# Performance work log

Hardware: AMD Instinct MI355X
Metric: run time of the kernel (lower is better)

The kernel has to match this reference:

```python
import jax, jax.numpy as jnp
import numpy as np

C_IN, C_OUT, KH, KW = 64, 128, 3, 3
STRIDE, PAD, DIL = 1, 1, 1
EPS = 1e-5


def setup_inputs() -> dict:
    key = jax.random.key(0)
    ks = jax.random.split(key, 7)
    B, H, W = 8, 112, 112
    x = jax.random.normal(ks[0], (B, C_IN, H, W), dtype=jnp.float32)
    # offset conv: produces 2*KH*KW offset channels; small init keeps offsets sane
    w_off = jax.random.normal(ks[1], (2 * KH * KW, C_IN, KH, KW), dtype=jnp.float32) * 0.01
    b_off = jax.random.normal(ks[2], (2 * KH * KW,), dtype=jnp.float32) * 0.01
    # deformable conv weight/bias
    fan_in = C_IN * KH * KW
    w_dcn = jax.random.normal(ks[3], (C_OUT, C_IN, KH, KW), dtype=jnp.float32) / np.sqrt(fan_in)
    b_dcn = jax.random.normal(ks[4], (C_OUT,), dtype=jnp.float32) * 0.01
    gamma = jnp.ones((C_OUT,), dtype=jnp.float32)
    beta = jnp.zeros((C_OUT,), dtype=jnp.float32)
    return {"x": x, "w_off": w_off, "b_off": b_off, "w_dcn": w_dcn,
            "b_dcn": b_dcn, "gamma": gamma, "beta": beta}


def _conv2d(x, w, b):
    y = jax.lax.conv_general_dilated(
        x, w, window_strides=(STRIDE, STRIDE),
        padding=((PAD, PAD), (PAD, PAD)),
        rhs_dilation=(DIL, DIL),
        dimension_numbers=("NCHW", "OIHW", "NCHW"))
    return y + b[None, :, None, None]


def _deform_conv(x, offset, w, b):
    # x: [B,C,H,W]; offset: [B, 2*KH*KW, Ho, Wo] with (dy, dx) pairs per tap
    B, C, H, W = x.shape
    KK = KH * KW
    Ho, Wo = offset.shape[2], offset.shape[3]
    off = offset.reshape(B, KK, 2, Ho, Wo)
    ky = (jnp.arange(KK) // KW).astype(jnp.float32)  # kernel row per tap
    kx = (jnp.arange(KK) % KW).astype(jnp.float32)
    base_y = (jnp.arange(Ho) * STRIDE - PAD).astype(jnp.float32)
    base_x = (jnp.arange(Wo) * STRIDE - PAD).astype(jnp.float32)
    # sampling positions [B, KK, Ho, Wo]
    py = off[:, :, 0] + base_y[None, None, :, None] + (ky * DIL)[None, :, None, None]
    px = off[:, :, 1] + base_x[None, None, None, :] + (kx * DIL)[None, :, None, None]

    y0 = jnp.floor(py)
    x0 = jnp.floor(px)
    wy1 = py - y0  # weight for y0+1
    wx1 = px - x0
    y0i = y0.astype(jnp.int32)
    x0i = x0.astype(jnp.int32)

    x_flat = x.reshape(B, C, H * W)

    def gather_corner(yi, xi, wgt):
        # yi, xi, wgt: [B, KK, Ho, Wo]
        valid = (yi >= 0) & (yi < H) & (xi >= 0) & (xi < W)
        idx = jnp.clip(yi, 0, H - 1) * W + jnp.clip(xi, 0, W - 1)
        idx = idx.reshape(B, -1)  # [B, KK*Ho*Wo]
        vals = jnp.take_along_axis(x_flat, idx[:, None, :], axis=2)  # [B, C, N]
        coef = (wgt * valid.astype(wgt.dtype)).reshape(B, 1, -1)
        return vals * coef

    samp = (gather_corner(y0i,     x0i,     (1 - wy1) * (1 - wx1))
            + gather_corner(y0i,     x0i + 1, (1 - wy1) * wx1)
            + gather_corner(y0i + 1, x0i,     wy1 * (1 - wx1))
            + gather_corner(y0i + 1, x0i + 1, wy1 * wx1))
    samp = samp.reshape(B, C, KK, Ho, Wo)
    out = jnp.einsum("bckhw,ock->bohw", samp, w.reshape(w.shape[0], C, KK))
    return out + b[None, :, None, None]


def reference(x, w_off, b_off, w_dcn, b_dcn, gamma, beta):
    offset = _conv2d(x, w_off, b_off)
    y = _deform_conv(x, offset, w_dcn, b_dcn)
    # BatchNorm2d (training mode: biased batch stats) + ReLU
    mean = jnp.mean(y, axis=(0, 2, 3))
    var = jnp.var(y, axis=(0, 2, 3))
    yhat = (y - mean[None, :, None, None]) * jax.lax.rsqrt(var + EPS)[None, :, None, None]
    y = gamma[None, :, None, None] * yhat + beta[None, :, None, None]
    return jax.nn.relu(y)
```

## Files before the change

kernel.cpp:

```cpp
#include <hip/hip_runtime.h>

#define H    112
#define W    112
#define HW   12544
#define CIN  64
#define COUT 128
#define BATCH 8
#define KK   9
#define OFFC 18
#define EPS  1e-5f
#define TP   32
#define KDIM 576
#define KHALF 288
#define KPAD2 296
#define NB   3136

typedef unsigned short ushort;
typedef unsigned int uint;
typedef _Float16 half2v __attribute__((ext_vector_type(2)));
typedef _Float16 half8  __attribute__((ext_vector_type(8)));
typedef __attribute__((ext_vector_type(4))) float floatx4;

__device__ __forceinline__ half2v u2h(uint u) {
  union { uint u; half2v h; } c; c.u = u; return c.h;
}
__device__ __forceinline__ uint h2u(half2v h) {
  union { uint u; half2v h; } c; c.h = h; return c.u;
}
__device__ __forceinline__ uint pack_h2(float a, float b) {
  half2v h; h[0] = (_Float16)a; h[1] = (_Float16)b; return h2u(h);
}
__device__ __forceinline__ ushort f2h_bits(float v) {
  union { _Float16 h; ushort u; } c; c.h = (_Float16)v; return c.u;
}

__global__ __launch_bounds__(256) void k_transpose_x(
    const float* __restrict__ x, ushort* __restrict__ xTh) {
  __shared__ float tile[64][65];
  int b = blockIdx.y;
  int p0 = blockIdx.x * 64;
  int tid = threadIdx.x;
  int j = tid & 63, cb = tid >> 6;
#pragma unroll
  for (int i = 0; i < 16; ++i) {
    int ci = cb * 16 + i;
    tile[ci][j] = x[((size_t)(b * CIN + ci)) * HW + p0 + j];
  }
  __syncthreads();
  int px = tid >> 2, ciq = tid & 3;
#pragma unroll
  for (int g = 0; g < 4; ++g) {
    int ci = ciq * 16 + g * 4;
    uint lo = pack_h2(tile[ci + 0][px], tile[ci + 1][px]);
    uint hi = pack_h2(tile[ci + 2][px], tile[ci + 3][px]);
    *(uint2*)&xTh[((size_t)b * HW + p0 + px) * 64 + ci] = make_uint2(lo, hi);
  }
}

__global__ __launch_bounds__(256) void k_prep_w(
    const float* __restrict__ w_off, const float* __restrict__ w_dcn,
    ushort* __restrict__ w_offT, ushort* __restrict__ w_mf) {
  int i = blockIdx.x * 256 + threadIdx.x;
  if (i < 32 * KDIM) {
    int oc = i / KDIM, k = i - oc * KDIM;
    int kk = k >> 6, ci = k & 63;
    float v = (oc < OFFC) ? w_off[(oc * CIN + ci) * KK + kk] : 0.f;
    w_offT[i] = f2h_bits(v);
  } else if (i < 32 * KDIM + COUT * KDIM) {
    int jj = i - 32 * KDIM;
    int co = jj / KDIM, k = jj - co * KDIM;
    int h = k / KHALF, r = k - h * KHALF;
    int kk = r >> 5, cil = r & 31;
    int ci = h * 32 + cil;
    w_mf[jj] = f2h_bits(w_dcn[(co * CIN + ci) * KK + kk]);
  }
}

__global__ __launch_bounds__(256) void k_offset_conv(
    const ushort* __restrict__ xTh, const ushort* __restrict__ w_offT,
    const float* __restrict__ bias, float* __restrict__ out) {
  int b = blockIdx.y;
  int wave = threadIdx.x >> 6, lane = threadIdx.x & 63;
  int row16 = lane & 15, quad = lane >> 4;
  int p = blockIdx.x * 64 + wave * 16 + row16;
  int ho = p / W, wo = p - ho * W;
  const ushort* xb = xTh + (size_t)b * HW * 64;

  half8 Bf[18];
#pragma unroll
  for (int ks = 0; ks < 18; ++ks) {
    int kk = ks >> 1;
    int ci0 = (ks & 1) * 32 + quad * 8;
    int kh = kk / 3, kw = kk - kh * 3;
    int yy = ho + kh - 1, xx = wo + kw - 1;
    bool valid = (yy >= 0) & (yy < H) & (xx >= 0) & (xx < W);
    half8 v = {0, 0, 0, 0, 0, 0, 0, 0};
    if (valid) v = *(const half8*)(xb + ((size_t)(yy * W + xx) << 6) + ci0);
    Bf[ks] = v;
  }
  floatx4 acc0 = {0.f, 0.f, 0.f, 0.f}, acc1 = acc0;
  const ushort* wa0 = w_offT + row16 * KDIM + quad * 8;
  const ushort* wa1 = w_offT + (16 + row16) * KDIM + quad * 8;
#pragma unroll
  for (int ks = 0; ks < 18; ++ks) {
    half8 A0 = *(const half8*)(wa0 + ks * 32);
    half8 A1 = *(const half8*)(wa1 + ks * 32);
    acc0 = __builtin_amdgcn_mfma_f32_16x16x32_f16(A0, Bf[ks], acc0, 0, 0, 0);
    acc1 = __builtin_amdgcn_mfma_f32_16x16x32_f16(A1, Bf[ks], acc1, 0, 0, 0);
  }
  float* ob = out + (size_t)b * OFFC * HW;
#pragma unroll
  for (int reg = 0; reg < 4; ++reg) {
    int oc = quad * 4 + reg;
    ob[(size_t)oc * HW + p] = acc0[reg] + bias[oc];
    int oc1 = 16 + oc;
    if (oc1 < OFFC) ob[(size_t)oc1 * HW + p] = acc1[reg] + bias[oc1];
  }
}

__global__ __launch_bounds__(256) void k_deform(
    const ushort* __restrict__ xTh, const float* __restrict__ off,
    const ushort* __restrict__ w_mf, float* __restrict__ y,
    float* __restrict__ psT) {
  __shared__ uint4  s_wh[KK][TP];
  __shared__ int4   s_i[KK][TP];
  __shared__ ushort samp[TP][KPAD2];

  int b = blockIdx.y;
  int p0 = blockIdx.x * TP;
  int bid = blockIdx.y * gridDim.x + blockIdx.x;
  int tid = threadIdx.x;
  const ushort* xb = xTh + (size_t)b * HW * 64;

  for (int it = tid; it < KK * TP; it += 256) {
    int kk = it >> 5;
    int px = it & 31;
    int p = p0 + px;
    int ho = p / W, wo = p - ho * W;
    float dy = off[((size_t)b * OFFC + 2 * kk) * HW + p];
    float dx = off[((size_t)b * OFFC + 2 * kk + 1) * HW + p];
    float py = dy + (float)(ho - 1 + kk / 3);
    float pxx = dx + (float)(wo - 1 + kk % 3);
    float y0f = floorf(py), x0f = floorf(pxx);
    float wy1 = py - y0f, wx1 = pxx - x0f;
    int y0 = (int)y0f, x0 = (int)x0f;
    int y1 = y0 + 1, x1 = x0 + 1;
    float vy0 = (y0 >= 0 && y0 < H) ? 1.f : 0.f;
    float vy1 = (y1 >= 0 && y1 < H) ? 1.f : 0.f;
    float vx0 = (x0 >= 0 && x0 < W) ? 1.f : 0.f;
    float vx1 = (x1 >= 0 && x1 < W) ? 1.f : 0.f;
    int cy0 = min(max(y0, 0), H - 1), cy1 = min(max(y1, 0), H - 1);
    int cx0 = min(max(x0, 0), W - 1), cx1 = min(max(x1, 0), W - 1);
    float w00 = (1.f - wy1) * (1.f - wx1) * vy0 * vx0;
    float w01 = (1.f - wy1) * wx1 * vy0 * vx1;
    float w10 = wy1 * (1.f - wx1) * vy1 * vx0;
    float w11 = wy1 * wx1 * vy1 * vx1;
    s_wh[kk][px] = make_uint4(pack_h2(w00, w00), pack_h2(w01, w01),
                              pack_h2(w10, w10), pack_h2(w11, w11));
    s_i[kk][px] = make_int4((cy0 * W + cx0) << 6, (cy0 * W + cx1) << 6,
                            (cy1 * W + cx0) << 6, (cy1 * W + cx1) << 6);
  }
  __syncthreads();

  int wave = tid >> 6, lane = tid & 63;
  int row16 = lane & 15, quad = lane >> 4;
  int koff = quad * 8;
  int co_base = wave * 32;
  const ushort* wa0 = w_mf + (size_t)(co_base + row16) * KDIM + koff;
  const ushort* wa1 = w_mf + (size_t)(co_base + 16 + row16) * KDIM + koff;

  floatx4 acc00 = {0.f, 0.f, 0.f, 0.f}, acc01 = acc00, acc10 = acc00, acc11 = acc00;

  for (int h = 0; h < 2; ++h) {
#pragma unroll
    for (int r = 0; r < 5; ++r) {
      int it = tid + r * 256;
      if (it < 1152) {
        int px = it / 36;
        int rem = it - px * 36;
        int kk = rem >> 2;
        int cig = rem & 3;
        int cil0 = cig * 8;
        int cio = h * 32 + cil0;
        uint4 wh = s_wh[kk][px];
        int4 iv = s_i[kk][px];
        half2v w0 = u2h(wh.x), w1 = u2h(wh.y), w2 = u2h(wh.z), w3 = u2h(wh.w);
        uint4 c0 = *(const uint4*)(xb + iv.x + cio);
        uint4 c1 = *(const uint4*)(xb + iv.y + cio);
        uint4 c2 = *(const uint4*)(xb + iv.z + cio);
        uint4 c3 = *(const uint4*)(xb + iv.w + cio);
        uint4 res;
        res.x = h2u(w0 * u2h(c0.x) + w1 * u2h(c1.x) + w2 * u2h(c2.x) + w3 * u2h(c3.x));
        res.y = h2u(w0 * u2h(c0.y) + w1 * u2h(c1.y) + w2 * u2h(c2.y) + w3 * u2h(c3.y));
        res.z = h2u(w0 * u2h(c0.z) + w1 * u2h(c1.z) + w2 * u2h(c2.z) + w3 * u2h(c3.z));
        res.w = h2u(w0 * u2h(c0.w) + w1 * u2h(c1.w) + w2 * u2h(c2.w) + w3 * u2h(c3.w));
        *(uint4*)&samp[px][kk * 32 + cil0] = res;
      }
    }
    __syncthreads();

    const ushort* sb0 = &samp[row16][koff];
    const ushort* sb1 = &samp[16 + row16][koff];
    const ushort* a0 = wa0 + h * KHALF;
    const ushort* a1 = wa1 + h * KHALF;
#pragma unroll
    for (int ks = 0; ks < 9; ++ks) {
      half8 A0 = *(const half8*)(a0 + ks * 32);
      half8 A1 = *(const half8*)(a1 + ks * 32);
      half8 B0 = *(const half8*)(sb0 + ks * 32);
      half8 B1 = *(const half8*)(sb1 + ks * 32);
      acc00 = __builtin_amdgcn_mfma_f32_16x16x32_f16(A0, B0, acc00, 0, 0, 0);
      acc01 = __builtin_amdgcn_mfma_f32_16x16x32_f16(A0, B1, acc01, 0, 0, 0);
      acc10 = __builtin_amdgcn_mfma_f32_16x16x32_f16(A1, B0, acc10, 0, 0, 0);
      acc11 = __builtin_amdgcn_mfma_f32_16x16x32_f16(A1, B1, acc11, 0, 0, 0);
    }
    if (h == 0) __syncthreads();
  }

  float* yb = y + (size_t)b * COUT * HW + p0;
#pragma unroll
  for (int reg = 0; reg < 4; ++reg) {
    int r0 = quad * 4 + reg;
    yb[(size_t)(co_base + r0) * HW + row16]      = acc00[reg];
    yb[(size_t)(co_base + r0) * HW + 16 + row16] = acc01[reg];
    yb[(size_t)(co_base + 16 + r0) * HW + row16]      = acc10[reg];
    yb[(size_t)(co_base + 16 + r0) * HW + 16 + row16] = acc11[reg];
  }
#pragma unroll
  for (int reg = 0; reg < 4; ++reg) {
    float s0 = acc00[reg] + acc01[reg];
    float q0 = acc00[reg] * acc00[reg] + acc01[reg] * acc01[reg];
    float s1 = acc10[reg] + acc11[reg];
    float q1 = acc10[reg] * acc10[reg] + acc11[reg] * acc11[reg];
#pragma unroll
    for (int m = 1; m < 16; m <<= 1) {
      s0 += __shfl_xor(s0, m, 64);
      q0 += __shfl_xor(q0, m, 64);
      s1 += __shfl_xor(s1, m, 64);
      q1 += __shfl_xor(q1, m, 64);
    }
    if (row16 == 0) {
      int c0 = co_base + quad * 4 + reg;
      int c1 = c0 + 16;
      psT[(size_t)c0 * NB + bid]         = s0;
      psT[(size_t)(128 + c0) * NB + bid] = q0;
      psT[(size_t)c1 * NB + bid]         = s1;
      psT[(size_t)(128 + c1) * NB + bid] = q1;
    }
  }
}

__global__ __launch_bounds__(256) void k_reduce(const float* __restrict__ psT,
                                                float* __restrict__ stats) {
  int j = blockIdx.x;
  int tid = threadIdx.x;
  float s = 0.f;
  for (int i = tid; i < NB; i += 256) s += psT[(size_t)j * NB + i];
#pragma unroll
  for (int o = 32; o > 0; o >>= 1) s += __shfl_down(s, o, 64);
  __shared__ float ls[4];
  int lane = tid & 63, wid = tid >> 6;
  if (lane == 0) ls[wid] = s;
  __syncthreads();
  if (tid == 0) stats[j] = ls[0] + ls[1] + ls[2] + ls[3];
}

__global__ __launch_bounds__(256) void k_norm(const float* __restrict__ y,
                                              const float* __restrict__ stats,
                                              const float* __restrict__ gamma,
                                              const float* __restrict__ beta,
                                              float* __restrict__ out) {
  int i4 = blockIdx.x * 256 + threadIdx.x;
  const int total4 = BATCH * COUT * HW / 4;
  if (i4 >= total4) return;
  size_t i = (size_t)i4 * 4;
  int c = (int)((i / HW) & (COUT - 1));
  const float N = (float)(BATCH * HW);
  float m = stats[c] / N;
  float var = stats[COUT + c] / N - m * m;
  float r = rsqrtf(var + EPS);
  float g = gamma[c], bt = beta[c];
  float4 v = *(const float4*)&y[i];
  v.x = fmaxf(0.f, (v.x - m) * r * g + bt);
  v.y = fmaxf(0.f, (v.y - m) * r * g + bt);
  v.z = fmaxf(0.f, (v.z - m) * r * g + bt);
  v.w = fmaxf(0.f, (v.w - m) * r * g + bt);
  *(float4*)&out[i] = v;
}

extern "C" void kernel_launch(void* const* d_in, const int* in_sizes, int n_in,
                              void* d_out, int out_size, void* d_ws, size_t ws_size,
                              hipStream_t stream) {
  const float* x     = (const float*)d_in[0];
  const float* w_off = (const float*)d_in[1];
  const float* b_off = (const float*)d_in[2];
  const float* w_dcn = (const float*)d_in[3];
  const float* gamma = (const float*)d_in[5];
  const float* beta  = (const float*)d_in[6];
  float* out = (float*)d_out;

  float* ws = (float*)d_ws;
  float*  off_buf = ws;
  float*  psT     = off_buf + 1806336;
  float*  stats   = psT + 802816;
  float*  y       = stats + 256;
  ushort* xTh     = (ushort*)(y + 12845056);
  ushort* w_mf    = xTh + 6422528;
  ushort* w_offT  = w_mf + 73728;

  k_transpose_x<<<dim3(HW / 64, BATCH), 256, 0, stream>>>(x, xTh);
  k_prep_w<<<(32 * KDIM + COUT * KDIM + 255) / 256, 256, 0, stream>>>(w_off, w_dcn, w_offT, w_mf);
  k_offset_conv<<<dim3(HW / 64, BATCH), 256, 0, stream>>>(xTh, w_offT, b_off, off_buf);
  k_deform<<<dim3(HW / TP, BATCH), 256, 0, stream>>>(xTh, off_buf, w_mf, y, psT);
  k_reduce<<<256, 256, 0, stream>>>(psT, stats);
  k_norm<<<(BATCH * COUT * HW / 4 + 255) / 256, 256, 0, stream>>>(y, stats, gamma, beta, out);
}
```

Measured before the change: 238.9 us.

## Store deform-conv output as fp16 via LDS-staged coalesced writes; restructure stats reduction

The deform kernel now stages its accumulator tile through shared memory, which is unioned with the sampling buffers, and writes the pre-norm activations as fp16 with vectorized coalesced stores instead of scattered fp32 stores. Per-block BN partial sums are also staged in shared memory and written contiguously. The reduce kernel now uses atomics over a block-major layout, which needs a memset of the stats buffer first. The norm kernel reads fp16 and processes eight elements per thread. This roughly halves intermediate traffic, at the cost of fp16 rounding of the pre-norm values and non-deterministic atomic summation order.

```diff
diff --git a/kernel.cpp b/kernel.cpp
--- a/kernel.cpp
+++ b/kernel.cpp
@@ -14,6 +14,7 @@
 #define KHALF 288
 #define KPAD2 296
 #define NB   3136
+#define YPAD 36
 
 typedef unsigned short ushort;
 typedef unsigned int uint;
@@ -32,6 +33,9 @@
 }
 __device__ __forceinline__ ushort f2h_bits(float v) {
   union { _Float16 h; ushort u; } c; c.h = (_Float16)v; return c.u;
+}
+__device__ __forceinline__ float h2f_bits(ushort u) {
+  union { ushort u; _Float16 h; } c; c.u = u; return (float)c.h;
 }
 
 __global__ __launch_bounds__(256) void k_transpose_x(
@@ -118,13 +122,15 @@
   }
 }
 
+struct SMemA { uint4 s_wh[KK][TP]; int4 s_i[KK][TP]; ushort samp[TP][KPAD2]; };
+struct SMemB { ushort yst[COUT][YPAD]; float stat_s[COUT]; float stat_q[COUT]; };
+union SMemU { SMemA a; SMemB b; };
+
 __global__ __launch_bounds__(256) void k_deform(
     const ushort* __restrict__ xTh, const float* __restrict__ off,
-    const ushort* __restrict__ w_mf, float* __restrict__ y,
+    const ushort* __restrict__ w_mf, ushort* __restrict__ y,
     float* __restrict__ psT) {
-  __shared__ uint4  s_wh[KK][TP];
-  __shared__ int4   s_i[KK][TP];
-  __shared__ ushort samp[TP][KPAD2];
+  __shared__ SMemU sm;
 
   int b = blockIdx.y;
   int p0 = blockIdx.x * TP;
@@ -155,10 +161,10 @@
     float w01 = (1.f - wy1) * wx1 * vy0 * vx1;
     float w10 = wy1 * (1.f - wx1) * vy1 * vx0;
     float w11 = wy1 * wx1 * vy1 * vx1;
-    s_wh[kk][px] = make_uint4(pack_h2(w00, w00), pack_h2(w01, w01),
-                              pack_h2(w10, w10), pack_h2(w11, w11));
-    s_i[kk][px] = make_int4((cy0 * W + cx0) << 6, (cy0 * W + cx1) << 6,
-                            (cy1 * W + cx0) << 6, (cy1 * W + cx1) << 6);
+    sm.a.s_wh[kk][px] = make_uint4(pack_h2(w00, w00), pack_h2(w01, w01),
+                                   pack_h2(w10, w10), pack_h2(w11, w11));
+    sm.a.s_i[kk][px] = make_int4((cy0 * W + cx0) << 6, (cy0 * W + cx1) << 6,
+                                 (cy1 * W + cx0) << 6, (cy1 * W + cx1) << 6);
   }
   __syncthreads();
 
@@ -182,8 +188,8 @@
         int cig = rem & 3;
         int cil0 = cig * 8;
         int cio = h * 32 + cil0;
-        uint4 wh = s_wh[kk][px];
-        int4 iv = s_i[kk][px];
+        uint4 wh = sm.a.s_wh[kk][px];
+        int4 iv = sm.a.s_i[kk][px];
         half2v w0 = u2h(wh.x), w1 = u2h(wh.y), w2 = u2h(wh.z), w3 = u2h(wh.w);
         uint4 c0 = *(const uint4*)(xb + iv.x + cio);
         uint4 c1 = *(const uint4*)(xb + iv.y + cio);
@@ -194,13 +200,13 @@
         res.y = h2u(w0 * u2h(c0.y) + w1 * u2h(c1.y) + w2 * u2h(c2.y) + w3 * u2h(c3.y));
         res.z = h2u(w0 * u2h(c0.z) + w1 * u2h(c1.z) + w2 * u2h(c2.z) + w3 * u2h(c3.z));
         res.w = h2u(w0 * u2h(c0.w) + w1 * u2h(c1.w) + w2 * u2h(c2.w) + w3 * u2h(c3.w));
-        *(uint4*)&samp[px][kk * 32 + cil0] = res;
+        *(uint4*)&sm.a.samp[px][kk * 32 + cil0] = res;
       }
     }
     __syncthreads();
 
-    const ushort* sb0 = &samp[row16][koff];
-    const ushort* sb1 = &samp[16 + row16][koff];
+    const ushort* sb0 = &sm.a.samp[row16][koff];
+    const ushort* sb1 = &sm.a.samp[16 + row16][koff];
     const ushort* a0 = wa0 + h * KHALF;
     const ushort* a1 = wa1 + h * KHALF;
 #pragma unroll
@@ -214,20 +220,17 @@
       acc10 = __builtin_amdgcn_mfma_f32_16x16x32_f16(A1, B0, acc10, 0, 0, 0);
       acc11 = __builtin_amdgcn_mfma_f32_16x16x32_f16(A1, B1, acc11, 0, 0, 0);
     }
-    if (h == 0) __syncthreads();
-  }
-
-  float* yb = y + (size_t)b * COUT * HW + p0;
+    __syncthreads();
+  }
+
 #pragma unroll
   for (int reg = 0; reg < 4; ++reg) {
-    int r0 = quad * 4 + reg;
-    yb[(size_t)(co_base + r0) * HW + row16]      = acc00[reg];
-    yb[(size_t)(co_base + r0) * HW + 16 + row16] = acc01[reg];
-    yb[(size_t)(co_base + 16 + r0) * HW + row16]      = acc10[reg];
-    yb[(size_t)(co_base + 16 + r0) * HW + 16 + row16] = acc11[reg];
-  }
-#pragma unroll
-  for (int reg = 0; reg < 4; ++reg) {
+    int cA = co_base + quad * 4 + reg;
+    int cB = cA + 16;
+    sm.b.yst[cA][row16]      = f2h_bits(acc00[reg]);
+    sm.b.yst[cA][16 + row16] = f2h_bits(acc01[reg]);
+    sm.b.yst[cB][row16]      = f2h_bits(acc10[reg]);
+    sm.b.yst[cB][16 + row16] = f2h_bits(acc11[reg]);
     float s0 = acc00[reg] + acc01[reg];
     float q0 = acc00[reg] * acc00[reg] + acc01[reg] * acc01[reg];
     float s1 = acc10[reg] + acc11[reg];
@@ -240,52 +243,68 @@
       q1 += __shfl_xor(q1, m, 64);
     }
     if (row16 == 0) {
-      int c0 = co_base + quad * 4 + reg;
-      int c1 = c0 + 16;
-      psT[(size_t)c0 * NB + bid]         = s0;
-      psT[(size_t)(128 + c0) * NB + bid] = q0;
-      psT[(size_t)c1 * NB + bid]         = s1;
-      psT[(size_t)(128 + c1) * NB + bid] = q1;
+      sm.b.stat_s[cA] = s0;
+      sm.b.stat_q[cA] = q0;
+      sm.b.stat_s[cB] = s1;
+      sm.b.stat_q[cB] = q1;
     }
+  }
+  __syncthreads();
+
+  {
+    int co = tid >> 1, seg = tid & 1;
+    const ushort* row = &sm.b.yst[co][seg * 16];
+    uint2 v0 = *(const uint2*)(row + 0);
+    uint2 v1 = *(const uint2*)(row + 4);
+    uint2 v2 = *(const uint2*)(row + 8);
+    uint2 v3 = *(const uint2*)(row + 12);
+    ushort* dst = y + (size_t)b * COUT * HW + (size_t)co * HW + p0 + seg * 16;
+    *(uint4*)dst       = make_uint4(v0.x, v0.y, v1.x, v1.y);
+    *(uint4*)(dst + 8) = make_uint4(v2.x, v2.y, v3.x, v3.y);
+    float sv = (tid < 128) ? sm.b.stat_s[tid] : sm.b.stat_q[tid - 128];
+    psT[(size_t)bid * 256 + tid] = sv;
   }
 }
 
 __global__ __launch_bounds__(256) void k_reduce(const float* __restrict__ psT,
                                                 float* __restrict__ stats) {
-  int j = blockIdx.x;
   int tid = threadIdx.x;
   float s = 0.f;
-  for (int i = tid; i < NB; i += 256) s += psT[(size_t)j * NB + i];
-#pragma unroll
-  for (int o = 32; o > 0; o >>= 1) s += __shfl_down(s, o, 64);
-  __shared__ float ls[4];
-  int lane = tid & 63, wid = tid >> 6;
-  if (lane == 0) ls[wid] = s;
-  __syncthreads();
-  if (tid == 0) stats[j] = ls[0] + ls[1] + ls[2] + ls[3];
-}
-
-__global__ __launch_bounds__(256) void k_norm(const float* __restrict__ y,
+  for (int i = blockIdx.x; i < NB; i += gridDim.x)
+    s += psT[(size_t)i * 256 + tid];
+  atomicAdd(&stats[tid], s);
+}
+
+__global__ __launch_bounds__(256) void k_norm(const ushort* __restrict__ y,
                                               const float* __restrict__ stats,
                                               const float* __restrict__ gamma,
                                               const float* __restrict__ beta,
                                               float* __restrict__ out) {
-  int i4 = blockIdx.x * 256 + threadIdx.x;
-  const int total4 = BATCH * COUT * HW / 4;
-  if (i4 >= total4) return;
-  size_t i = (size_t)i4 * 4;
+  int i8 = blockIdx.x * 256 + threadIdx.x;
+  const int total8 = BATCH * COUT * HW / 8;
+  if (i8 >= total8) return;
+  size_t i = (size_t)i8 * 8;
   int c = (int)((i / HW) & (COUT - 1));
   const float N = (float)(BATCH * HW);
   float m = stats[c] / N;
   float var = stats[COUT + c] / N - m * m;
   float r = rsqrtf(var + EPS);
   float g = gamma[c], bt = beta[c];
-  float4 v = *(const float4*)&y[i];
-  v.x = fmaxf(0.f, (v.x - m) * r * g + bt);
-  v.y = fmaxf(0.f, (v.y - m) * r * g + bt);
-  v.z = fmaxf(0.f, (v.z - m) * r * g + bt);
-  v.w = fmaxf(0.f, (v.w - m) * r * g + bt);
-  *(float4*)&out[i] = v;
+  float a = r * g;
+  float base = bt - m * a;
+  uint4 u = *(const uint4*)&y[i];
+  float4 o0, o1;
+  half2v h0 = u2h(u.x), h1 = u2h(u.y), h2 = u2h(u.z), h3 = u2h(u.w);
+  o0.x = fmaxf(0.f, fmaf((float)h0[0], a, base));
+  o0.y = fmaxf(0.f, fmaf((float)h0[1], a, base));
+  o0.z = fmaxf(0.f, fmaf((float)h1[0], a, base));
+  o0.w = fmaxf(0.f, fmaf((float)h1[1], a, base));
+  o1.x = fmaxf(0.f, fmaf((float)h2[0], a, base));
+  o1.y = fmaxf(0.f, fmaf((float)h2[1], a, base));
+  o1.z = fmaxf(0.f, fmaf((float)h3[0], a, base));
+  o1.w = fmaxf(0.f, fmaf((float)h3[1], a, base));
+  *(float4*)&out[i]     = o0;
+  *(float4*)&out[i + 4] = o1;
 }
 
 extern "C" void kernel_launch(void* const* d_in, const int* in_sizes, int n_in,
@@ -303,15 +322,16 @@
   float*  off_buf = ws;
   float*  psT     = off_buf + 1806336;
   float*  stats   = psT + 802816;
-  float*  y       = stats + 256;
-  ushort* xTh     = (ushort*)(y + 12845056);
+  ushort* xTh     = (ushort*)(stats + 256);
   ushort* w_mf    = xTh + 6422528;
   ushort* w_offT  = w_mf + 73728;
-
+  ushort* y_h     = w_offT + 18432;
+
+  hipMemsetAsync(stats, 0, 256 * sizeof(float), stream);
   k_transpose_x<<<dim3(HW / 64, BATCH), 256, 0, stream>>>(x, xTh);
   k_prep_w<<<(32 * KDIM + COUT * KDIM + 255) / 256, 256, 0, stream>>>(w_off, w_dcn, w_offT, w_mf);
   k_offset_conv<<<dim3(HW / 64, BATCH), 256, 0, stream>>>(xTh, w_offT, b_off, off_buf);
-  k_deform<<<dim3(HW / TP, BATCH), 256, 0, stream>>>(xTh, off_buf, w_mf, y, psT);
-  k_reduce<<<256, 256, 0, stream>>>(psT, stats);
-  k_norm<<<(BATCH * COUT * HW / 4 + 255) / 256, 256, 0, stream>>>(y, stats, gamma, beta, out);
-}
+  k_deform<<<dim3(HW / TP, BATCH), 256, 0, stream>>>(xTh, off_buf, w_mf, y_h, psT);
+  k_reduce<<<64, 256, 0, stream>>>(psT, stats);
+  k_norm<<<(BATCH * COUT * HW / 8 + 255) / 256, 256, 0, stream>>>(y_h, stats, gamma, beta, out);
+}
```

Measured after the change: 243.0 us. Within noise of the previous version (+1.7%).
